# Performance work log

Hardware: AMD Instinct MI355X
Metric: run time of the kernel (lower is better)

Reference implementation:

```python
import jax, jax.numpy as jnp
import numpy as np

B, S = 4, 2000            # meshes, nodes per mesh
N = B * S                  # total nodes
E = 32000                  # directed edges (before self loops)
H_TR, D_TR, FF, TOUT = 4, 64, 2048, 16
HID, HEADS, HC = 512, 6, 512
DEFORM_IN, NUM_LOOP = 7, 3


def setup_inputs():
    key = jax.random.key(0)
    ks = iter(jax.random.split(key, 64))
    def W(shape):
        return jax.random.normal(next(ks), shape, jnp.float32) / np.sqrt(shape[-1])
    inp = {}
    inp['conv_feat'] = jax.random.normal(next(ks), (B, 1), jnp.float32)
    inp['mesh_feat'] = jax.random.normal(next(ks), (N, 4), jnp.float32)
    inp['x'] = jax.random.normal(next(ks), (N, DEFORM_IN), jnp.float32)
    inp['edge_index'] = jax.random.randint(next(ks), (2, E), 0, N, jnp.int32)
    inp['embed_w'] = W((D_TR, 4)); inp['embed_b'] = jnp.zeros((D_TR,), jnp.float32)
    inp['in_proj_w'] = W((3 * D_TR, D_TR)); inp['in_proj_b'] = jnp.zeros((3 * D_TR,), jnp.float32)
    inp['out_proj_w'] = W((D_TR, D_TR)); inp['out_proj_b'] = jnp.zeros((D_TR,), jnp.float32)
    inp['ln1_g'] = jnp.ones((D_TR,), jnp.float32); inp['ln1_b'] = jnp.zeros((D_TR,), jnp.float32)
    inp['ln2_g'] = jnp.ones((D_TR,), jnp.float32); inp['ln2_b'] = jnp.zeros((D_TR,), jnp.float32)
    inp['ff1_w'] = W((FF, D_TR)); inp['ff1_b'] = jnp.zeros((FF,), jnp.float32)
    inp['ff2_w'] = W((D_TR, FF)); inp['ff2_b'] = jnp.zeros((D_TR,), jnp.float32)
    inp['tout_w'] = W((TOUT, D_TR)); inp['tout_b'] = jnp.zeros((TOUT,), jnp.float32)
    all_feat = DEFORM_IN - 2 + TOUT  # 21
    inp['lin_w'] = W((HID, all_feat)); inp['lin_b'] = jnp.zeros((HID,), jnp.float32)
    gin = 2 + HID  # 514
    inp['gat_wl'] = W((HEADS * HC, gin)); inp['gat_bl'] = jnp.zeros((HEADS * HC,), jnp.float32)
    inp['gat_wr'] = W((HEADS * HC, gin)); inp['gat_br'] = jnp.zeros((HEADS * HC,), jnp.float32)
    inp['gat_att'] = jax.random.normal(next(ks), (HEADS, HC), jnp.float32) / np.sqrt(HC)
    inp['gat_bias'] = jnp.zeros((HC,), jnp.float32)
    inp['coord1_w'] = W((HID // 2, HID)); inp['coord1_b'] = jnp.zeros((HID // 2,), jnp.float32)
    inp['coord2_w'] = W((2, HID // 2)); inp['coord2_b'] = jnp.zeros((2,), jnp.float32)
    return inp


def _ln(h, g, b):
    m = jnp.mean(h, -1, keepdims=True)
    v = jnp.var(h, -1, keepdims=True)
    return (h - m) / jnp.sqrt(v + 1e-5) * g + b


def _mrt_forward(conv_feat, mesh_feat, x, edge_index, embed_w, embed_b, in_proj_w, in_proj_b,
                 out_proj_w, out_proj_b, ln1_g, ln1_b, ln2_g, ln2_b, ff1_w, ff1_b, ff2_w, ff2_b,
                 tout_w, tout_b, lin_w, lin_b, gat_wl, gat_bl, gat_wr, gat_br, gat_att, gat_bias,
                 coord1_w, coord1_b, coord2_w, coord2_b):
    bsz = conv_feat.shape[0]
    feat_dim = mesh_feat.shape[-1]
    # ---- transformer encoder (1 post-norm layer, eval mode => no dropout) ----
    h = mesh_feat.reshape(bsz, -1, feat_dim) @ embed_w.T + embed_b  # [B,S,D]
    qkv = h @ in_proj_w.T + in_proj_b
    q, k, v = jnp.split(qkv, 3, axis=-1)
    dh = D_TR // H_TR
    hd = lambda t: t.reshape(bsz, -1, H_TR, dh)
    attn = jax.nn.softmax(jnp.einsum('bqhd,bkhd->bhqk', hd(q), hd(k)) / np.sqrt(dh), axis=-1)
    o = jnp.einsum('bhqk,bkhd->bqhd', attn, hd(v)).reshape(bsz, -1, D_TR)
    h = _ln(h + (o @ out_proj_w.T + out_proj_b), ln1_g, ln1_b)
    ff = jax.nn.relu(h @ ff1_w.T + ff1_b) @ ff2_w.T + ff2_b
    h = _ln(h + ff, ln2_g, ln2_b)
    feats = (h @ tout_w.T + tout_b).reshape(-1, TOUT)               # [N,16]
    feats = jnp.concatenate([x[:, 2:], feats], axis=1)             # [N,21]
    hidden = jax.nn.selu(feats @ lin_w.T + lin_b)                  # [N,512]
    # ---- recurrent GATv2 deformer loop ----
    coord = x[:, :2]
    n = x.shape[0]
    loops = jnp.arange(n, dtype=edge_index.dtype)                  # self loops (GATv2Conv default)
    src = jnp.concatenate([edge_index[0], loops])
    dst = jnp.concatenate([edge_index[1], loops])
    for _ in range(NUM_LOOP):
        inp = jnp.concatenate([coord, hidden], axis=1)             # [N,514]
        xl = (inp @ gat_wl.T + gat_bl).reshape(n, HEADS, HC)
        xr = (inp @ gat_wr.T + gat_br).reshape(n, HEADS, HC)
        e = jax.nn.leaky_relu(xl[src] + xr[dst], 0.2)              # [Etot,H,C]
        logits = jnp.einsum('ehc,hc->eh', e, gat_att)              # [Etot,H]
        mx = jax.ops.segment_max(logits, dst, num_segments=n)
        a = jnp.exp(logits - mx[dst])
        a = a / jax.ops.segment_sum(a, dst, num_segments=n)[dst]   # softmax per dst node
        agg = jax.ops.segment_sum(xl[src] * a[:, :, None], dst, num_segments=n)  # [N,H,C]
        hidden = jax.nn.selu(jnp.mean(agg, axis=1) + gat_bias)     # concat=False => head mean
        coord = jax.nn.selu(hidden @ coord1_w.T + coord1_b) @ coord2_w.T + coord2_b
    return coord


def reference(conv_feat, mesh_feat, x, edge_index, embed_w, embed_b, in_proj_w, in_proj_b,
              out_proj_w, out_proj_b, ln1_g, ln1_b, ln2_g, ln2_b, ff1_w, ff1_b, ff2_w, ff2_b,
              tout_w, tout_b, lin_w, lin_b, gat_wl, gat_bl, gat_wr, gat_br, gat_att, gat_bias,
              coord1_w, coord1_b, coord2_w, coord2_b):
    return _mrt_forward(conv_feat, mesh_feat, x, edge_index, embed_w, embed_b, in_proj_w, in_proj_b,
                        out_proj_w, out_proj_b, ln1_g, ln1_b, ln2_g, ln2_b, ff1_w, ff1_b, ff2_w, ff2_b,
                        tout_w, tout_b, lin_w, lin_b, gat_wl, gat_bl, gat_wr, gat_br, gat_att, gat_bias,
                        coord1_w, coord1_b, coord2_w, coord2_b)
```

## Files before the change

### kernel.cpp

```cpp
#include <hip/hip_runtime.h>
#include <hip/hip_bf16.h>
#include <math.h>

#define NN     8000
#define MPAD   8064
#define BATCH  4
#define SEQ    2000
#define DTR    64
#define NHTR   4
#define DHD    16
#define FFD    2048
#define TOUTD  16
#define HIDD   512
#define NHEADS 6
#define HCD    512
#define GIND   514
#define GOUT   3072
#define GOUT2  6144
#define NEDGE  32000
#define ELOOP  40000

#define K1     576
#define K2     1152

#define KSPLIT 20
#define KCH    100

#define CDIV(a,b) (((a)+(b)-1)/(b))

using bf16x8 = __attribute__((__ext_vector_type__(8))) __bf16;
using f32x4  = __attribute__((__ext_vector_type__(4))) float;

__device__ __forceinline__ float selu_f(float x){
  const float a = 1.6732632423543772848f;
  const float s = 1.0507009873554805f;
  return x > 0.f ? s * x : s * a * (__expf(x) - 1.f);
}

__device__ __forceinline__ unsigned short f2bf_rn(float x){
  unsigned u = __float_as_uint(x);
  unsigned r = (u + 0x7fffu + ((u >> 16) & 1u)) >> 16;
  return (unsigned short)r;
}
__device__ __forceinline__ float bf2f(unsigned short h){
  return __uint_as_float((unsigned)h << 16);
}

template<int ACT>
__global__ __launch_bounds__(256) void k_gemm(const float* __restrict__ A,
    const float* __restrict__ W, const float* __restrict__ bias,
    float* __restrict__ C, int M, int N, int K)
{
  __shared__ float As[16][68];
  __shared__ float Ws[16][68];
  const int tid = threadIdx.x;
  const int bm = blockIdx.y * 64, bn = blockIdx.x * 64;
  const int tx = tid & 15, ty = tid >> 4;
  float acc[4][4] = {};
  for (int k0 = 0; k0 < K; k0 += 16){
    #pragma unroll
    for (int i = 0; i < 4; ++i){
      int el = tid + (i << 8);
      int kk = el & 15, r = el >> 4;
      int gk = k0 + kk;
      int gm = bm + r;
      As[kk][r] = (gm < M && gk < K) ? A[(size_t)gm * K + gk] : 0.f;
      int gn = bn + r;
      Ws[kk][r] = (gn < N && gk < K) ? W[(size_t)gn * K + gk] : 0.f;
    }
    __syncthreads();
    #pragma unroll
    for (int kk = 0; kk < 16; ++kk){
      float av[4], wv[4];
      #pragma unroll
      for (int i = 0; i < 4; ++i) av[i] = As[kk][ty*4+i];
      #pragma unroll
      for (int j = 0; j < 4; ++j) wv[j] = Ws[kk][tx*4+j];
      #pragma unroll
      for (int i = 0; i < 4; ++i)
        #pragma unroll
        for (int j = 0; j < 4; ++j) acc[i][j] = fmaf(av[i], wv[j], acc[i][j]);
    }
    __syncthreads();
  }
  #pragma unroll
  for (int i = 0; i < 4; ++i){
    int gm = bm + ty*4 + i;
    if (gm >= M) continue;
    #pragma unroll
    for (int j = 0; j < 4; ++j){
      int gn = bn + tx*4 + j;
      if (gn >= N) continue;
      float v = acc[i][j] + bias[gn];
      if (ACT == 1) v = fmaxf(v, 0.f);
      if (ACT == 2) v = selu_f(v);
      C[(size_t)gm * N + gn] = v;
    }
  }
}

__global__ __launch_bounds__(256) void k_addln4(const float* __restrict__ x,
    const float* __restrict__ part, const float* __restrict__ bias,
    const float* __restrict__ g, const float* __restrict__ b,
    float* __restrict__ out)
{
  int row = blockIdx.x * 4 + (threadIdx.x >> 6);
  int lane = threadIdx.x & 63;
  if (row >= NN) return;
  float y = bias[lane];
  #pragma unroll
  for (int z = 0; z < 4; ++z) y += part[(size_t)z*NN*DTR + (size_t)row*64 + lane];
  float v = x[(size_t)row*64 + lane] + y;
  float s1 = v, s2 = v * v;
  #pragma unroll
  for (int o = 32; o; o >>= 1){ s1 += __shfl_xor(s1, o); s2 += __shfl_xor(s2, o); }
  float mean = s1 * (1.f/64.f);
  float var  = s2 * (1.f/64.f) - mean * mean;
  float r = rsqrtf(var + 1e-5f);
  out[(size_t)row*64 + lane] = (v - mean) * r * g[lane] + b[lane];
}

__global__ __launch_bounds__(256) void k_coord2(const float* __restrict__ c1,
    const float* __restrict__ w2, const float* __restrict__ b2,
    float* __restrict__ out, short* __restrict__ abf)
{
  int n = blockIdx.x, t = threadIdx.x;
  float v = c1[(size_t)n*256 + t];
  float d0 = v * w2[t], d1 = v * w2[256 + t];
  #pragma unroll
  for (int o = 32; o; o >>= 1){ d0 += __shfl_xor(d0, o); d1 += __shfl_xor(d1, o); }
  __shared__ float red[8];
  int wv = t >> 6;
  if ((t & 63) == 0){ red[wv] = d0; red[4 + wv] = d1; }
  __syncthreads();
  if (t < 2){
    float c = (t == 0 ? red[0]+red[1]+red[2]+red[3] + b2[0]
                      : red[4]+red[5]+red[6]+red[7] + b2[1]);
    out[(size_t)n*2 + t] = c;
    abf[(size_t)n*K2 + t] = (short)f2bf_rn(c);
  }
}

__global__ void k_cvt_w(const float* __restrict__ W, short* __restrict__ Wbf)
{
  int i = blockIdx.x * blockDim.x + threadIdx.x;
  if (i >= GOUT * K1) return;
  int n = i / K1, k = i - K1 * n;
  float v = (k < GIND) ? W[(size_t)n * GIND + k] : 0.f;
  Wbf[i] = (short)f2bf_rn(v);
}

__global__ void k_cvt_wc(const float* __restrict__ W, short* __restrict__ Wbf)
{
  int i = blockIdx.x * blockDim.x + threadIdx.x;
  if (i >= 256 * K1) return;
  int n = i / K1, k = i - K1 * n;
  float v = (k >= 2 && k < GIND) ? W[(size_t)n * HIDD + (k - 2)] : 0.f;
  Wbf[i] = (short)f2bf_rn(v);
}

__global__ void k_cvt_w1(const float* __restrict__ W, short* __restrict__ Wbf)
{
  int i = blockIdx.x * blockDim.x + threadIdx.x;
  if (i >= FFD * 64) return;
  Wbf[i] = (short)f2bf_rn(W[i]);
}

__global__ void k_cvt_w2(const float* __restrict__ W, short* __restrict__ Wbf)
{
  int i = blockIdx.x * blockDim.x + threadIdx.x;
  if (i >= 128 * FFD) return;
  int n = i / FFD;
  Wbf[i] = (short)f2bf_rn(n < 64 ? W[i] : 0.f);
}

__global__ void k_cvt_h(const float* __restrict__ h, short* __restrict__ hbf)
{
  int i = blockIdx.x * blockDim.x + threadIdx.x;
  if (i >= MPAD * 64) return;
  int n = i >> 6;
  hbf[i] = (short)f2bf_rn(n < NN ? h[i] : 0.f);
}

__global__ void k_cvt_a(const float* __restrict__ coord,
                        const float* __restrict__ hidden,
                        short* __restrict__ Abf)
{
  int i = blockIdx.x * blockDim.x + threadIdx.x;
  if (i >= MPAD * K1) return;
  int n = i / K1, k = i - K1 * n;
  float v = 0.f;
  if (n < NN && k < GIND)
    v = (k < 2) ? coord[(size_t)n*2 + k] : hidden[(size_t)n*HIDD + k - 2];
  Abf[(size_t)n * K2 + k] = (short)f2bf_rn(v);
}

__global__ void k_wfuse(const float* __restrict__ ipw, const float* __restrict__ ipb,
                        const float* __restrict__ ew, const float* __restrict__ eb,
                        float* __restrict__ Wp, float* __restrict__ bp)
{
  int c = blockIdx.x * blockDim.x + threadIdx.x;
  if (c >= 192) return;
  float w4[4] = {0.f, 0.f, 0.f, 0.f};
  float bb = 0.f;
  for (int d = 0; d < 64; ++d){
    float wq = ipw[c*64 + d];
    #pragma unroll
    for (int j = 0; j < 4; ++j) w4[j] = fmaf(wq, ew[d*4 + j], w4[j]);
    bb = fmaf(wq, eb[d], bb);
  }
  #pragma unroll
  for (int j = 0; j < 4; ++j) Wp[c*4 + j] = w4[j];
  bp[c] = bb + ipb[c];
}

__global__ __launch_bounds__(256) void k_embqkv(const float* __restrict__ mesh,
    const float* __restrict__ ew, const float* __restrict__ eb,
    const float* __restrict__ Wp, const float* __restrict__ bp,
    float* __restrict__ h, float* __restrict__ qkv)
{
  int n = blockIdx.x, t = threadIdx.x;
  float m0 = mesh[n*4+0], m1 = mesh[n*4+1], m2 = mesh[n*4+2], m3 = mesh[n*4+3];
  if (t < 64){
    const float* wr = ew + t*4;
    h[(size_t)n*64 + t] =
      fmaf(m0, wr[0], fmaf(m1, wr[1], fmaf(m2, wr[2], m3*wr[3]))) + eb[t];
  } else {
    int c = t - 64;
    const float* wr = Wp + c*4;
    qkv[(size_t)n*192 + c] =
      fmaf(m0, wr[0], fmaf(m1, wr[1], fmaf(m2, wr[2], m3*wr[3]))) + bp[c];
  }
}

__global__ __launch_bounds__(256) void k_gat_mfma(
    const short* __restrict__ Abf, const short* __restrict__ Wbf,
    const float* __restrict__ bl, const float* __restrict__ br,
    unsigned short* __restrict__ Cb)
{
  __shared__ __align__(16) short smem[2 * 128 * 64];
  short* As = smem;
  short* Bs = smem + 128 * 64;
  const int tid  = threadIdx.x;
  int lin = blockIdx.y * 48 + blockIdx.x;
  int xcd = lin & 7;
  int idx = lin >> 3;
  int nb  = xcd * 6 + idx % 6;
  int mb  = idx / 6;
  const int bm = mb * 128, bn = nb * 128;
  const int w    = tid >> 6, lane = tid & 63;
  const int wr   = w >> 1, wc = w & 1;
  const int lrow = lane & 15;

  f32x4 acc[4][4];
  #pragma unroll
  for (int i = 0; i < 4; ++i)
    #pragma unroll
    for (int j = 0; j < 4; ++j) acc[i][j] = (f32x4){0.f, 0.f, 0.f, 0.f};

  for (int kt = 0; kt < 9; ++kt){
    int koff = kt * 64;
    __syncthreads();
    #pragma unroll
    for (int i = 0; i < 4; ++i){
      int l  = i * 256 + tid;
      int r  = l >> 3, j = l & 7;
      int js = j ^ (r & 7);
      const short* ga = Abf + (size_t)(bm + r) * K2 + koff + js * 8;
      const short* gb = Wbf + (size_t)(bn + r) * K1 + koff + js * 8;
      short* la = As + ((i * 256 + w * 64) << 3);
      short* lb = Bs + ((i * 256 + w * 64) << 3);
      __builtin_amdgcn_global_load_lds(
          (const __attribute__((address_space(1))) unsigned*)ga,
          (__attribute__((address_space(3))) unsigned*)la, 16, 0, 0);
      __builtin_amdgcn_global_load_lds(
          (const __attribute__((address_space(1))) unsigned*)gb,
          (__attribute__((address_space(3))) unsigned*)lb, 16, 0, 0);
    }
    __syncthreads();
    #pragma unroll
    for (int ks = 0; ks < 2; ++ks){
      const int co = ((ks * 4 + (lane >> 4)) ^ (lrow & 7)) * 8;
      bf16x8 fa[4], fb[4];
      #pragma unroll
      for (int mi = 0; mi < 4; ++mi)
        fa[mi] = *(const bf16x8*)&As[(wr*64 + mi*16 + lrow) * 64 + co];
      #pragma unroll
      for (int ni = 0; ni < 4; ++ni)
        fb[ni] = *(const bf16x8*)&Bs[(wc*64 + ni*16 + lrow) * 64 + co];
      #pragma unroll
      for (int mi = 0; mi < 4; ++mi)
        #pragma unroll
        for (int ni = 0; ni < 4; ++ni)
          acc[mi][ni] = __builtin_amdgcn_mfma_f32_16x16x32_bf16(
              fa[mi], fb[ni], acc[mi][ni], 0, 0, 0);
    }
  }
  __syncthreads();
  unsigned short* Ct = (unsigned short*)smem;
  #pragma unroll
  for (int mi = 0; mi < 4; ++mi){
    #pragma unroll
    for (int ni = 0; ni < 4; ++ni){
      int col = wc*64 + ni*16 + lrow;
      int gn  = bn + col;
      float bv = (gn < GOUT) ? bl[gn] : br[gn - GOUT];
      #pragma unroll
      for (int j = 0; j < 4; ++j){
        int row  = wr*64 + mi*16 + (lane >> 4)*4 + j;
        int colp = col ^ (((row >> 2) & 3) << 4);
        Ct[row*128 + colp] = f2bf_rn(acc[mi][ni][j] + bv);
      }
    }
  }
  __syncthreads();
  #pragma unroll
  for (int c = 0; c < 8; ++c){
    int g   = c*256 + tid;
    int row = g >> 4, cc = g & 15;
    int ccp = cc ^ (((row >> 2) & 3) << 1);
    int gm  = bm + row;
    if (gm < NN){
      bf16x8 v = *(const bf16x8*)&Ct[row*128 + ccp*8];
      *(bf16x8*)&Cb[(size_t)gm * GOUT2 + bn + cc*8] = v;
    }
  }
}

__global__ __launch_bounds__(256) void k_c1_mfma(
    const short* __restrict__ Abf, const short* __restrict__ Wbf,
    const float* __restrict__ c1b, float* __restrict__ C)
{
  __shared__ __align__(16) short smem[2 * 128 * 64];
  short* As = smem;
  short* Bs = smem + 128 * 64;
  const int tid  = threadIdx.x;
  const int bm = blockIdx.y * 128, bn = blockIdx.x * 128;
  const int w    = tid >> 6, lane = tid & 63;
  const int wr   = w >> 1, wc = w & 1;
  const int lrow = lane & 15;

  f32x4 acc[4][4];
  #pragma unroll
  for (int i = 0; i < 4; ++i)
    #pragma unroll
    for (int j = 0; j < 4; ++j) acc[i][j] = (f32x4){0.f, 0.f, 0.f, 0.f};

  for (int kt = 0; kt < 9; ++kt){
    int koff = kt * 64;
    __syncthreads();
    #pragma unroll
    for (int i = 0; i < 4; ++i){
      int l  = i * 256 + tid;
      int r  = l >> 3, j = l & 7;
      int js = j ^ (r & 7);
      const short* ga = Abf + (size_t)(bm + r) * K2 + koff + js * 8;
      const short* gb = Wbf + (size_t)(bn + r) * K1 + koff + js * 8;
      short* la = As + ((i * 256 + w * 64) << 3);
      short* lb = Bs + ((i * 256 + w * 64) << 3);
      __builtin_amdgcn_global_load_lds(
          (const __attribute__((address_space(1))) unsigned*)ga,
          (__attribute__((address_space(3))) unsigned*)la, 16, 0, 0);
      __builtin_amdgcn_global_load_lds(
          (const __attribute__((address_space(1))) unsigned*)gb,
          (__attribute__((address_space(3))) unsigned*)lb, 16, 0, 0);
    }
    __syncthreads();
    #pragma unroll
    for (int ks = 0; ks < 2; ++ks){
      const int co = ((ks * 4 + (lane >> 4)) ^ (lrow & 7)) * 8;
      bf16x8 fa[4], fb[4];
      #pragma unroll
      for (int mi = 0; mi < 4; ++mi)
        fa[mi] = *(const bf16x8*)&As[(wr*64 + mi*16 + lrow) * 64 + co];
      #pragma unroll
      for (int ni = 0; ni < 4; ++ni)
        fb[ni] = *(const bf16x8*)&Bs[(wc*64 + ni*16 + lrow) * 64 + co];
      #pragma unroll
      for (int mi = 0; mi < 4; ++mi)
        #pragma unroll
        for (int ni = 0; ni < 4; ++ni)
          acc[mi][ni] = __builtin_amdgcn_mfma_f32_16x16x32_bf16(
              fa[mi], fb[ni], acc[mi][ni], 0, 0, 0);
    }
  }
  #pragma unroll
  for (int mi = 0; mi < 4; ++mi){
    #pragma unroll
    for (int ni = 0; ni < 4; ++ni){
      int gn = bn + wc*64 + ni*16 + lrow;
      float bv = c1b[gn];
      #pragma unroll
      for (int j = 0; j < 4; ++j){
        int gm = bm + wr*64 + mi*16 + (lane >> 4) * 4 + j;
        if (gm < NN)
          C[(size_t)gm * 256 + gn] = selu_f(acc[mi][ni][j] + bv);
      }
    }
  }
}

__global__ __launch_bounds__(256) void k_ff1_mfma(
    const short* __restrict__ hbf, const short* __restrict__ w1b,
    const float* __restrict__ b1, unsigned short* __restrict__ Cb)
{
  __shared__ __align__(16) short smem[2 * 128 * 64];
  short* As = smem;
  short* Bs = smem + 128 * 64;
  const int tid  = threadIdx.x;
  const int bm = blockIdx.y * 128, bn = blockIdx.x * 128;
  const int w    = tid >> 6, lane = tid & 63;
  const int wr   = w >> 1, wc = w & 1;
  const int lrow = lane & 15;

  f32x4 acc[4][4];
  #pragma unroll
  for (int i = 0; i < 4; ++i)
    #pragma unroll
    for (int j = 0; j < 4; ++j) acc[i][j] = (f32x4){0.f, 0.f, 0.f, 0.f};

  #pragma unroll
  for (int i = 0; i < 4; ++i){
    int l  = i * 256 + tid;
    int r  = l >> 3, j = l & 7;
    int js = j ^ (r & 7);
    const short* ga = hbf + (size_t)(bm + r) * 64 + js * 8;
    const short* gb = w1b + (size_t)(bn + r) * 64 + js * 8;
    short* la = As + ((i * 256 + w * 64) << 3);
    short* lb = Bs + ((i * 256 + w * 64) << 3);
    __builtin_amdgcn_global_load_lds(
        (const __attribute__((address_space(1))) unsigned*)ga,
        (__attribute__((address_space(3))) unsigned*)la, 16, 0, 0);
    __builtin_amdgcn_global_load_lds(
        (const __attribute__((address_space(1))) unsigned*)gb,
        (__attribute__((address_space(3))) unsigned*)lb, 16, 0, 0);
  }
  __syncthreads();
  #pragma unroll
  for (int ks = 0; ks < 2; ++ks){
    const int co = ((ks * 4 + (lane >> 4)) ^ (lrow & 7)) * 8;
    bf16x8 fa[4], fb[4];
    #pragma unroll
    for (int mi = 0; mi < 4; ++mi)
      fa[mi] = *(const bf16x8*)&As[(wr*64 + mi*16 + lrow) * 64 + co];
    #pragma unroll
    for (int ni = 0; ni < 4; ++ni)
      fb[ni] = *(const bf16x8*)&Bs[(wc*64 + ni*16 + lrow) * 64 + co];
    #pragma unroll
    for (int mi = 0; mi < 4; ++mi)
      #pragma unroll
      for (int ni = 0; ni < 4; ++ni)
        acc[mi][ni] = __builtin_amdgcn_mfma_f32_16x16x32_bf16(
            fa[mi], fb[ni], acc[mi][ni], 0, 0, 0);
  }
  __syncthreads();
  unsigned short* Ct = (unsigned short*)smem;
  #pragma unroll
  for (int mi = 0; mi < 4; ++mi){
    #pragma unroll
    for (int ni = 0; ni < 4; ++ni){
      int col = wc*64 + ni*16 + lrow;
      int gn  = bn + col;
      float bv = b1[gn];
      #pragma unroll
      for (int j = 0; j < 4; ++j){
        int row  = wr*64 + mi*16 + (lane >> 4)*4 + j;
        int colp = col ^ (((row >> 2) & 3) << 4);
        Ct[row*128 + colp] = f2bf_rn(fmaxf(acc[mi][ni][j] + bv, 0.f));
      }
    }
  }
  __syncthreads();
  #pragma unroll
  for (int c = 0; c < 8; ++c){
    int g   = c*256 + tid;
    int row = g >> 4, cc = g & 15;
    int ccp = cc ^ (((row >> 2) & 3) << 1);
    int gm  = bm + row;
    if (gm < NN){
      bf16x8 v = *(const bf16x8*)&Ct[row*128 + ccp*8];
      *(bf16x8*)&Cb[(size_t)gm * FFD + bn + cc*8] = v;
    }
  }
}

__global__ __launch_bounds__(256) void k_ff2_mfma(
    const unsigned short* __restrict__ ffb, const short* __restrict__ w2b,
    float* __restrict__ part)
{
  __shared__ __align__(16) short smem[2 * 128 * 64];
  short* As = smem;
  short* Bs = smem + 128 * 64;
  const int tid  = threadIdx.x;
  const int bm = blockIdx.y * 128;
  const int kz = blockIdx.z;
  const int w    = tid >> 6, lane = tid & 63;
  const int wr   = w >> 1, wc = w & 1;
  const int lrow = lane & 15;

  f32x4 acc[4][4];
  #pragma unroll
  for (int i = 0; i < 4; ++i)
    #pragma unroll
    for (int j = 0; j < 4; ++j) acc[i][j] = (f32x4){0.f, 0.f, 0.f, 0.f};

  for (int kt = 0; kt < 8; ++kt){
    int koff = kz * 512 + kt * 64;
    __syncthreads();
    #pragma unroll
    for (int i = 0; i < 4; ++i){
      int l  = i * 256 + tid;
      int r  = l >> 3, j = l & 7;
      int js = j ^ (r & 7);
      const short* ga = (const short*)ffb + (size_t)(bm + r) * FFD + koff + js * 8;
      const short* gb = w2b + (size_t)r * FFD + koff + js * 8;
      short* la = As + ((i * 256 + w * 64) << 3);
      short* lb = Bs + ((i * 256 + w * 64) << 3);
      __builtin_amdgcn_global_load_lds(
          (const __attribute__((address_space(1))) unsigned*)ga,
          (__attribute__((address_space(3))) unsigned*)la, 16, 0, 0);
      __builtin_amdgcn_global_load_lds(
          (const __attribute__((address_space(1))) unsigned*)gb,
          (__attribute__((address_space(3))) unsigned*)lb, 16, 0, 0);
    }
    __syncthreads();
    #pragma unroll
    for (int ks = 0; ks < 2; ++ks){
      const int co = ((ks * 4 + (lane >> 4)) ^ (lrow & 7)) * 8;
      bf16x8 fa[4], fb[4];
      #pragma unroll
      for (int mi = 0; mi < 4; ++mi)
        fa[mi] = *(const bf16x8*)&As[(wr*64 + mi*16 + lrow) * 64 + co];
      #pragma unroll
      for (int ni = 0; ni < 4; ++ni)
        fb[ni] = *(const bf16x8*)&Bs[(wc*64 + ni*16 + lrow) * 64 + co];
      #pragma unroll
      for (int mi = 0; mi < 4; ++mi)
        #pragma unroll
        for (int ni = 0; ni < 4; ++ni)
          acc[mi][ni] = __builtin_amdgcn_mfma_f32_16x16x32_bf16(
              fa[mi], fb[ni], acc[mi][ni], 0, 0, 0);
    }
  }
  if (wc == 0){
    float* pz = part + (size_t)kz * NN * 64;
    #pragma unroll
    for (int mi = 0; mi < 4; ++mi){
      #pragma unroll
      for (int ni = 0; ni < 4; ++ni){
        int gn = ni*16 + lrow;
        #pragma unroll
        for (int j = 0; j < 4; ++j){
          int gm = bm + wr*64 + mi*16 + (lane >> 4) * 4 + j;
          if (gm < NN)
            pz[(size_t)gm * 64 + gn] = acc[mi][ni][j];
        }
      }
    }
  }
}

__global__ __launch_bounds__(128) void k_attn_part(const float* __restrict__ qkv,
    float* __restrict__ Pm, float* __restrict__ Pl, float* __restrict__ Pacc)
{
  __shared__ float Ks[KCH][DHD];
  __shared__ float Vs[KCH][DHD];
  const int q1 = blockIdx.x * 128 + threadIdx.x;
  const int q2 = q1 + 1024;
  const int bh = blockIdx.y;
  const int b  = bh >> 2, h = bh & 3;
  const int ks = blockIdx.z;
  const bool v2 = q2 < SEQ;
  const float SC = 0.25f * 1.4426950408889634f;
  float qv1[DHD], qv2[DHD];
  {
    const float4* qr = (const float4*)(qkv + ((size_t)(b*SEQ + q1))*192 + h*DHD);
    #pragma unroll
    for (int j = 0; j < 4; ++j){
      float4 t = qr[j];
      qv1[j*4+0] = t.x; qv1[j*4+1] = t.y; qv1[j*4+2] = t.z; qv1[j*4+3] = t.w;
    }
  }
  if (v2){
    const float4* qr = (const float4*)(qkv + ((size_t)(b*SEQ + q2))*192 + h*DHD);
    #pragma unroll
    for (int j = 0; j < 4; ++j){
      float4 t = qr[j];
      qv2[j*4+0] = t.x; qv2[j*4+1] = t.y; qv2[j*4+2] = t.z; qv2[j*4+3] = t.w;
    }
  } else {
    #pragma unroll
    for (int j = 0; j < DHD; ++j) qv2[j] = 0.f;
  }
  const int kbeg = ks * KCH;
  for (int el = threadIdx.x; el < KCH * 4; el += 128){
    int r = el >> 2, d4 = el & 3;
    const float4* base = (const float4*)(qkv + ((size_t)(b*SEQ + kbeg + r))*192 + h*DHD);
    ((float4*)Ks[r])[d4] = base[16 + d4];
    ((float4*)Vs[r])[d4] = base[32 + d4];
  }
  __syncthreads();
  float m1 = -1e30f, l1 = 0.f, a1[DHD] = {};
  float m2 = -1e30f, l2 = 0.f, a2[DHD] = {};
  for (int r = 0; r < KCH; ++r){
    float s1 = 0.f, s2 = 0.f;
    #pragma unroll
    for (int d = 0; d < DHD; ++d){
      float kd = Ks[r][d];
      s1 = fmaf(qv1[d], kd, s1);
      s2 = fmaf(qv2[d], kd, s2);
    }
    s1 *= SC; s2 *= SC;
    if (__any((s1 > m1 + 8.f) || (s2 > m2 + 8.f))){
      float mn1 = fmaxf(m1, s1), mn2 = fmaxf(m2, s2);
      float c1 = exp2f(m1 - mn1), c2 = exp2f(m2 - mn2);
      l1 *= c1; l2 *= c2;
      #pragma unroll
      for (int d = 0; d < DHD; ++d){ a1[d] *= c1; a2[d] *= c2; }
      m1 = mn1; m2 = mn2;
    }
    float p1 = exp2f(s1 - m1), p2 = exp2f(s2 - m2);
    l1 += p1; l2 += p2;
    #pragma unroll
    for (int d = 0; d < DHD; ++d){
      float vd = Vs[r][d];
      a1[d] = fmaf(p1, vd, a1[d]);
      a2[d] = fmaf(p2, vd, a2[d]);
    }
  }
  {
    size_t qi = ((size_t)bh * SEQ + q1) * KSPLIT + ks;
    Pm[qi] = m1; Pl[qi] = l1;
    #pragma unroll
    for (int d = 0; d < DHD; ++d) Pacc[qi*DHD + d] = a1[d];
  }
  if (v2){
    size_t qi = ((size_t)bh * SEQ + q2) * KSPLIT + ks;
    Pm[qi] = m2; Pl[qi] = l2;
    #pragma unroll
    for (int d = 0; d < DHD; ++d) Pacc[qi*DHD + d] = a2[d];
  }
}

__global__ void k_attn_comb(const float* __restrict__ Pm, const float* __restrict__ Pl,
                            const float* __restrict__ Pacc, float* __restrict__ o)
{
  int qi = blockIdx.x * blockDim.x + threadIdx.x;
  if (qi >= BATCH * NHTR * SEQ) return;
  float m = -1e30f;
  #pragma unroll
  for (int ks = 0; ks < KSPLIT; ++ks) m = fmaxf(m, Pm[(size_t)qi*KSPLIT + ks]);
  float l = 0.f, acc[DHD] = {};
  #pragma unroll
  for (int ks = 0; ks < KSPLIT; ++ks){
    size_t p = (size_t)qi*KSPLIT + ks;
    float sc = exp2f(Pm[p] - m);
    l += Pl[p] * sc;
    #pragma unroll
    for (int d = 0; d < DHD; ++d) acc[d] = fmaf(Pacc[p*DHD + d], sc, acc[d]);
  }
  int bh = qi / SEQ, q = qi - bh * SEQ;
  int b = bh >> 2, h = bh & 3;
  float inv = 1.f / l;
  #pragma unroll
  for (int d = 0; d < DHD; ++d)
    o[((size_t)(b*SEQ + q))*64 + h*DHD + d] = acc[d] * inv;
}

__global__ __launch_bounds__(256) void k_addln(const float* __restrict__ x,
    const float* __restrict__ y, const float* __restrict__ g,
    const float* __restrict__ b, float* __restrict__ out)
{
  int row = blockIdx.x * 4 + (threadIdx.x >> 6);
  int lane = threadIdx.x & 63;
  if (row >= NN) return;
  float v = x[(size_t)row*64 + lane] + y[(size_t)row*64 + lane];
  float s1 = v, s2 = v * v;
  #pragma unroll
  for (int o = 32; o; o >>= 1){ s1 += __shfl_xor(s1, o); s2 += __shfl_xor(s2, o); }
  float mean = s1 * (1.f/64.f);
  float var  = s2 * (1.f/64.f) - mean * mean;
  float r = rsqrtf(var + 1e-5f);
  out[(size_t)row*64 + lane] = (v - mean) * r * g[lane] + b[lane];
}

__global__ void k_prep(const float* __restrict__ x, const float* __restrict__ tout,
                       float* __restrict__ feats, float* __restrict__ coord)
{
  int i = blockIdx.x * blockDim.x + threadIdx.x;
  if (i >= NN * 23) return;
  int n = i / 23, c = i - 23*n;
  if (c < 21)
    feats[(size_t)n*21 + c] = (c < 5) ? x[(size_t)n*7 + 2 + c] : tout[(size_t)n*16 + c - 5];
  else
    coord[(size_t)n*2 + (c - 21)] = x[(size_t)n*7 + (c - 21)];
}

__global__ void k_count(const int* __restrict__ dst, int* __restrict__ cnt)
{
  int e = blockIdx.x * blockDim.x + threadIdx.x;
  if (e >= ELOOP) return;
  int d = (e < NEDGE) ? dst[e] : e - NEDGE;
  atomicAdd(&cnt[d], 1);
}

__global__ __launch_bounds__(1024) void k_scan(const int* __restrict__ cnt,
                                               int* __restrict__ ptr)
{
  __shared__ int part[1024];
  int tid = threadIdx.x;
  const int per = 8;
  int loc[per]; int s = 0;
  int base = tid * per;
  #pragma unroll
  for (int i = 0; i < per; ++i){
    int v = (base + i < NN) ? cnt[base + i] : 0;
    loc[i] = s; s += v;
  }
  part[tid] = s;
  __syncthreads();
  for (int off = 1; off < 1024; off <<= 1){
    int v = 0;
    if (tid >= off) v = part[tid - off];
    __syncthreads();
    if (tid >= off) part[tid] += v;
    __syncthreads();
  }
  int pre = tid ? part[tid - 1] : 0;
  #pragma unroll
  for (int i = 0; i < per; ++i)
    if (base + i < NN) ptr[base + i] = pre + loc[i];
  if (tid == 1023) ptr[NN] = part[1023];
}

__global__ void k_fill(const int* __restrict__ dst, const int* __restrict__ ptr,
                       int* __restrict__ fil, int* __restrict__ eid)
{
  int e = blockIdx.x * blockDim.x + threadIdx.x;
  if (e >= ELOOP) return;
  int d = (e < NEDGE) ? dst[e] : e - NEDGE;
  int pos = ptr[d] + atomicAdd(&fil[d], 1);
  eid[pos] = e;
}

__global__ __launch_bounds__(256) void k_logits(const unsigned short* __restrict__ xc,
    const int* __restrict__ src_a, const int* __restrict__ dst_a,
    const int* __restrict__ eid, const float* __restrict__ att,
    float* __restrict__ logits2)
{
  int bid = blockIdx.x;
  int wgs = (bid & 7) * 1250 + (bid >> 3);
  int pos = wgs * 4 + (threadIdx.x >> 6);
  if (pos >= ELOOP) return;
  int lane = threadIdx.x & 63;
  int e = eid[pos];
  int s = (e < NEDGE) ? src_a[e] : e - NEDGE;
  int d = (e < NEDGE) ? dst_a[e] : e - NEDGE;
  const uint4* pl = (const uint4*)(xc + (size_t)s * GOUT2);
  const uint4* pr = (const uint4*)(xc + (size_t)d * GOUT2 + GOUT);
  const float4* pa = (const float4*)att;
  #pragma unroll 2
  for (int h = 0; h < NHEADS; ++h){
    uint4 ua = pl[h*64 + lane];
    uint4 ub = pr[h*64 + lane];
    float4 w0 = pa[h*128 + lane*2], w1 = pa[h*128 + lane*2 + 1];
    float acc = 0.f;
    auto pair = [&](unsigned a, unsigned b, float wl, float wh){
      float vl = __uint_as_float(a << 16)        + __uint_as_float(b << 16);
      float vh = __uint_as_float(a & 0xffff0000u)+ __uint_as_float(b & 0xffff0000u);
      vl = vl > 0.f ? vl : 0.2f * vl;
      vh = vh > 0.f ? vh : 0.2f * vh;
      acc = fmaf(vl, wl, acc);
      acc = fmaf(vh, wh, acc);
    };
    pair(ua.x, ub.x, w0.x, w0.y);
    pair(ua.y, ub.y, w0.z, w0.w);
    pair(ua.z, ub.z, w1.x, w1.y);
    pair(ua.w, ub.w, w1.z, w1.w);
    #pragma unroll
    for (int o2 = 32; o2; o2 >>= 1) acc += __shfl_xor(acc, o2);
    if (lane == 0) logits2[pos*NHEADS + h] = acc;
  }
}

__global__ void k_stats(const float* __restrict__ logits2, const int* __restrict__ ptr,
                        float* __restrict__ mx, float* __restrict__ inv)
{
  int i = blockIdx.x * blockDim.x + threadIdx.x;
  if (i >= NN * NHEADS) return;
  int n = i / NHEADS, h = i - NHEADS * n;
  int s0 = ptr[n], s1 = ptr[n + 1];
  float m = -1e30f;
  for (int t = s0; t < s1; ++t) m = fmaxf(m, logits2[t*NHEADS + h]);
  float s = 0.f;
  for (int t = s0; t < s1; ++t) s += __expf(logits2[t*NHEADS + h] - m);
  mx[i] = m; inv[i] = 1.f / s;
}

__global__ __launch_bounds__(256) void k_agg(const unsigned short* __restrict__ xc,
    const float* __restrict__ logits2, const float* __restrict__ mx,
    const float* __restrict__ inv, const int* __restrict__ ptr,
    const int* __restrict__ eid, const int* __restrict__ src_a,
    const float* __restrict__ gbias, float* __restrict__ hidden,
    short* __restrict__ abf)
{
  const int n = blockIdx.x;
  const int tid = threadIdx.x;
  __shared__ float a_sh[64 * NHEADS];
  __shared__ int src_sh[64];
  const int s0 = ptr[n];
  const int deg = ptr[n + 1] - s0;
  float acc[12] = {};
  for (int base = 0; base < deg; base += 64){
    int cnt = min(64, deg - base);
    __syncthreads();
    for (int t = tid; t < cnt * NHEADS; t += 256){
      int ei = t / NHEADS, h = t - NHEADS * ei;
      a_sh[t] = __expf(logits2[(s0 + base + ei)*NHEADS + h] - mx[n*NHEADS + h])
                * inv[n*NHEADS + h];
      if (h == 0){
        int e = eid[s0 + base + ei];
        src_sh[ei] = (e < NEDGE) ? src_a[e] : e - NEDGE;
      }
    }
    __syncthreads();
    for (int i2 = 0; i2 < cnt; ++i2){
      const unsigned* row = (const unsigned*)(xc + (size_t)src_sh[i2] * GOUT2);
      #pragma unroll
      for (int k = 0; k < NHEADS; ++k){
        unsigned u = row[tid + (k << 8)];
        float wgt = a_sh[i2*NHEADS + k];
        acc[2*k]   = fmaf(__uint_as_float(u << 16),         wgt, acc[2*k]);
        acc[2*k+1] = fmaf(__uint_as_float(u & 0xffff0000u), wgt, acc[2*k+1]);
      }
    }
  }
  float m0 = (acc[0]+acc[2]+acc[4]+acc[6]+acc[8]+acc[10]) * (1.f/6.f);
  float m1 = (acc[1]+acc[3]+acc[5]+acc[7]+acc[9]+acc[11]) * (1.f/6.f);
  float2 out;
  out.x = selu_f(m0 + gbias[2*tid]);
  out.y = selu_f(m1 + gbias[2*tid + 1]);
  *(float2*)&hidden[(size_t)n*HIDD + 2*tid] = out;
  unsigned short h0 = f2bf_rn(out.x), h1 = f2bf_rn(out.y);
  *(unsigned*)&abf[(size_t)n*K2 + 2 + 2*tid] = (unsigned)h0 | ((unsigned)h1 << 16);
}

extern "C" void kernel_launch(void* const* d_in, const int* in_sizes, int n_in,
                              void* d_out, int out_size, void* d_ws, size_t ws_size,
                              hipStream_t stream)
{
  const float* mesh     = (const float*)d_in[1];
  const float* xin      = (const float*)d_in[2];
  const int*   ei       = (const int*)d_in[3];
  const float* embed_w  = (const float*)d_in[4];
  const float* embed_b  = (const float*)d_in[5];
  const float* in_proj_w= (const float*)d_in[6];
  const float* in_proj_b= (const float*)d_in[7];
  const float* out_proj_w=(const float*)d_in[8];
  const float* out_proj_b=(const float*)d_in[9];
  const float* ln1_g    = (const float*)d_in[10];
  const float* ln1_b    = (const float*)d_in[11];
  const float* ln2_g    = (const float*)d_in[12];
  const float* ln2_b    = (const float*)d_in[13];
  const float* ff1_w    = (const float*)d_in[14];
  const float* ff1_b    = (const float*)d_in[15];
  const float* ff2_w    = (const float*)d_in[16];
  const float* ff2_b    = (const float*)d_in[17];
  const float* tout_w   = (const float*)d_in[18];
  const float* tout_b   = (const float*)d_in[19];
  const float* lin_w    = (const float*)d_in[20];
  const float* lin_b    = (const float*)d_in[21];
  const float* gat_wl   = (const float*)d_in[22];
  const float* gat_bl   = (const float*)d_in[23];
  const float* gat_wr   = (const float*)d_in[24];
  const float* gat_br   = (const float*)d_in[25];
  const float* gat_att  = (const float*)d_in[26];
  const float* gat_bias = (const float*)d_in[27];
  const float* coord1_w = (const float*)d_in[28];
  const float* coord1_b = (const float*)d_in[29];
  const float* coord2_w = (const float*)d_in[30];
  const float* coord2_b = (const float*)d_in[31];

  const int* esrc = ei;
  const int* edst = ei + NEDGE;

  char* ws = (char*)d_ws;
  size_t off = 0;
  auto alloc = [&](size_t nbytes){
    size_t o = off; off += (nbytes + 255) & ~(size_t)255; return o;
  };
  float* hidden = (float*)(ws + alloc((size_t)NN * HIDD * 4));
  float* coord  = (float*)(ws + alloc((size_t)NN * 2 * 4));
  unsigned short* xc = (unsigned short*)(ws + alloc((size_t)NN * GOUT2 * 2));
  float* logits = (float*)(ws + alloc((size_t)ELOOP * NHEADS * 4));
  float* mxb    = (float*)(ws + alloc((size_t)NN * NHEADS * 4));
  float* invb   = (float*)(ws + alloc((size_t)NN * NHEADS * 4));
  int*   ptr    = (int*)(ws + alloc((size_t)(NN + 1) * 4));
  int*   eid    = (int*)(ws + alloc((size_t)ELOOP * 4));
  int*   cnt    = (int*)(ws + alloc((size_t)NN * 4));
  int*   fil    = (int*)(ws + alloc((size_t)NN * 4));
  short* abf    = (short*)(ws + alloc((size_t)MPAD * K2 * 2));
  short* wlbf   = (short*)(ws + alloc((size_t)GOUT * K1 * 2));
  short* wrbf   = (short*)(ws + alloc((size_t)GOUT * K1 * 2));
  short* wcb    = (short*)(ws + alloc((size_t)256 * K1 * 2));
  short* w1b    = (short*)(ws + alloc((size_t)FFD * 64 * 2));
  short* w2b    = (short*)(ws + alloc((size_t)128 * FFD * 2));
  short* hbf    = (short*)(ws + alloc((size_t)MPAD * 64 * 2));
  float* c1     = (float*)(ws + alloc((size_t)NN * 256 * 4));
  float* Wp     = (float*)(ws + alloc((size_t)192 * 4 * 4));
  float* bp     = (float*)(ws + alloc((size_t)192 * 4));

  char* arena = (char*)xc;
  float* h       = (float*)(arena + ((size_t)0  << 20));
  float* o       = (float*)(arena + ((size_t)2  << 20));
  float* tmp     = (float*)(arena + ((size_t)4  << 20));
  float* feats   = (float*)(arena + ((size_t)6  << 20));
  float* toutb   = (float*)(arena + ((size_t)7  << 20));
  float* qkv     = (float*)(arena + ((size_t)8  << 20));
  float* Pm      = (float*)(arena + ((size_t)15 << 20));
  float* Pl      = (float*)(arena + ((size_t)18 << 20));
  float* Pacc    = (float*)(arena + ((size_t)21 << 20));
  unsigned short* ffb = (unsigned short*)(arena + ((size_t)28 << 20));
  float* part_f2 = (float*)(arena + ((size_t)62 << 20));

  k_wfuse<<<1, 192, 0, stream>>>(in_proj_w, in_proj_b, embed_w, embed_b, Wp, bp);
  k_cvt_w1<<<CDIV(FFD*64, 256), 256, 0, stream>>>(ff1_w, w1b);
  k_cvt_w2<<<CDIV(128*FFD, 256), 256, 0, stream>>>(ff2_w, w2b);
  hipMemsetAsync(cnt, 0, (size_t)NN * 4, stream);
  hipMemsetAsync(fil, 0, (size_t)NN * 4, stream);
  k_count<<<CDIV(ELOOP, 256), 256, 0, stream>>>(edst, cnt);
  k_scan<<<1, 1024, 0, stream>>>(cnt, ptr);
  k_fill<<<CDIV(ELOOP, 256), 256, 0, stream>>>(edst, ptr, fil, eid);
  k_cvt_w<<<CDIV(GOUT*K1, 256), 256, 0, stream>>>(gat_wl, wlbf);
  k_cvt_w<<<CDIV(GOUT*K1, 256), 256, 0, stream>>>(gat_wr, wrbf);
  k_cvt_wc<<<CDIV(256*K1, 256), 256, 0, stream>>>(coord1_w, wcb);

  k_embqkv<<<NN, 256, 0, stream>>>(mesh, embed_w, embed_b, Wp, bp, h, qkv);
  k_attn_part<<<dim3(CDIV(SEQ,256), BATCH*NHTR, KSPLIT), 128, 0, stream>>>(qkv, Pm, Pl, Pacc);
  k_attn_comb<<<CDIV(BATCH*NHTR*SEQ, 256), 256, 0, stream>>>(Pm, Pl, Pacc, o);
  k_gemm<0><<<dim3(1, CDIV(NN,64)), 256, 0, stream>>>(o, out_proj_w, out_proj_b, tmp, NN, 64, 64);
  k_addln<<<CDIV(NN,4), 256, 0, stream>>>(h, tmp, ln1_g, ln1_b, h);
  k_cvt_h<<<CDIV(MPAD*64, 256), 256, 0, stream>>>(h, hbf);
  k_ff1_mfma<<<dim3(16, 63), 256, 0, stream>>>(hbf, w1b, ff1_b, ffb);
  k_ff2_mfma<<<dim3(1, 63, 4), 256, 0, stream>>>(ffb, w2b, part_f2);
  k_addln4<<<CDIV(NN,4), 256, 0, stream>>>(h, part_f2, ff2_b, ln2_g, ln2_b, h);
  k_gemm<0><<<dim3(1, CDIV(NN,64)), 256, 0, stream>>>(h, tout_w, tout_b, toutb, NN, TOUTD, DTR);
  k_prep<<<CDIV(NN*23, 256), 256, 0, stream>>>(xin, toutb, feats, coord);
  k_gemm<2><<<dim3(CDIV(HIDD,64), CDIV(NN,64)), 256, 0, stream>>>(feats, lin_w, lin_b, hidden, NN, HIDD, 21);
  k_cvt_a<<<CDIV(MPAD*K1, 256), 256, 0, stream>>>(coord, hidden, abf);

  for (int it = 0; it < 3; ++it){
    k_gat_mfma<<<dim3(48, 63), 256, 0, stream>>>(abf, wlbf, gat_bl, gat_br, xc);
    k_logits<<<ELOOP/4, 256, 0, stream>>>(xc, esrc, edst, eid, gat_att, logits);
    k_stats<<<CDIV(NN*NHEADS, 256), 256, 0, stream>>>(logits, ptr, mxb, invb);
    k_agg<<<NN, 256, 0, stream>>>(xc, logits, mxb, invb, ptr, eid, esrc, gat_bias, hidden, abf);
    k_c1_mfma<<<dim3(2, 63), 256, 0, stream>>>(abf, wcb, coord1_b, c1);
    float* cdst = (it == 2) ? (float*)d_out : coord;
    k_coord2<<<NN, 256, 0, stream>>>(c1, coord2_w, coord2_b, cdst, abf);
  }
}
```

Before: 801.6 us.

## Fuse GAT logits, softmax stats and aggregation into one online-softmax kernel

Replaces the three GAT kernels (edge logits, per-node max/sum stats, weighted aggregation) with a single per-destination-node kernel. It computes logits on the fly from the gathered source row and the resident dst row, then applies an online softmax. This removes the logits, max and inverse-sum intermediate buffers, two launches per iteration and the second read of source rows. The cost is two block-wide barriers per edge for the cross-wave logit reduction, which serialises work inside each block. Separately, the bf16 conversion of h is folded into the first add+layernorm, and the padding rows are zeroed once.

```diff
diff --git a/kernel.cpp b/kernel.cpp
--- a/kernel.cpp
+++ b/kernel.cpp
@@ -174,14 +174,6 @@
   Wbf[i] = (short)f2bf_rn(n < 64 ? W[i] : 0.f);
 }
 
-__global__ void k_cvt_h(const float* __restrict__ h, short* __restrict__ hbf)
-{
-  int i = blockIdx.x * blockDim.x + threadIdx.x;
-  if (i >= MPAD * 64) return;
-  int n = i >> 6;
-  hbf[i] = (short)f2bf_rn(n < NN ? h[i] : 0.f);
-}
-
 __global__ void k_cvt_a(const float* __restrict__ coord,
                         const float* __restrict__ hidden,
                         short* __restrict__ Abf)
@@ -669,7 +661,8 @@
 
 __global__ __launch_bounds__(256) void k_addln(const float* __restrict__ x,
     const float* __restrict__ y, const float* __restrict__ g,
-    const float* __restrict__ b, float* __restrict__ out)
+    const float* __restrict__ b, float* __restrict__ out,
+    short* __restrict__ hbf)
 {
   int row = blockIdx.x * 4 + (threadIdx.x >> 6);
   int lane = threadIdx.x & 63;
@@ -681,7 +674,9 @@
   float mean = s1 * (1.f/64.f);
   float var  = s2 * (1.f/64.f) - mean * mean;
   float r = rsqrtf(var + 1e-5f);
-  out[(size_t)row*64 + lane] = (v - mean) * r * g[lane] + b[lane];
+  float res = (v - mean) * r * g[lane] + b[lane];
+  out[(size_t)row*64 + lane] = res;
+  hbf[(size_t)row*64 + lane] = (short)f2bf_rn(res);
 }
 
 __global__ void k_prep(const float* __restrict__ x, const float* __restrict__ tout,
@@ -696,6 +691,13 @@
     coord[(size_t)n*2 + (c - 21)] = x[(size_t)n*7 + (c - 21)];
 }
 
+__global__ void k_zpad(short* __restrict__ hbf)
+{
+  int i = blockIdx.x * blockDim.x + threadIdx.x;
+  if (i >= (MPAD - NN) * 64) return;
+  hbf[(size_t)NN*64 + i] = 0;
+}
+
 __global__ void k_count(const int* __restrict__ dst, int* __restrict__ cnt)
 {
   int e = blockIdx.x * blockDim.x + threadIdx.x;
@@ -743,103 +745,90 @@
   eid[pos] = e;
 }
 
-__global__ __launch_bounds__(256) void k_logits(const unsigned short* __restrict__ xc,
-    const int* __restrict__ src_a, const int* __restrict__ dst_a,
-    const int* __restrict__ eid, const float* __restrict__ att,
-    float* __restrict__ logits2)
-{
-  int bid = blockIdx.x;
-  int wgs = (bid & 7) * 1250 + (bid >> 3);
-  int pos = wgs * 4 + (threadIdx.x >> 6);
-  if (pos >= ELOOP) return;
-  int lane = threadIdx.x & 63;
-  int e = eid[pos];
-  int s = (e < NEDGE) ? src_a[e] : e - NEDGE;
-  int d = (e < NEDGE) ? dst_a[e] : e - NEDGE;
-  const uint4* pl = (const uint4*)(xc + (size_t)s * GOUT2);
-  const uint4* pr = (const uint4*)(xc + (size_t)d * GOUT2 + GOUT);
-  const float4* pa = (const float4*)att;
-  #pragma unroll 2
-  for (int h = 0; h < NHEADS; ++h){
-    uint4 ua = pl[h*64 + lane];
-    uint4 ub = pr[h*64 + lane];
-    float4 w0 = pa[h*128 + lane*2], w1 = pa[h*128 + lane*2 + 1];
-    float acc = 0.f;
-    auto pair = [&](unsigned a, unsigned b, float wl, float wh){
-      float vl = __uint_as_float(a << 16)        + __uint_as_float(b << 16);
-      float vh = __uint_as_float(a & 0xffff0000u)+ __uint_as_float(b & 0xffff0000u);
-      vl = vl > 0.f ? vl : 0.2f * vl;
-      vh = vh > 0.f ? vh : 0.2f * vh;
-      acc = fmaf(vl, wl, acc);
-      acc = fmaf(vh, wh, acc);
-    };
-    pair(ua.x, ub.x, w0.x, w0.y);
-    pair(ua.y, ub.y, w0.z, w0.w);
-    pair(ua.z, ub.z, w1.x, w1.y);
-    pair(ua.w, ub.w, w1.z, w1.w);
-    #pragma unroll
-    for (int o2 = 32; o2; o2 >>= 1) acc += __shfl_xor(acc, o2);
-    if (lane == 0) logits2[pos*NHEADS + h] = acc;
-  }
-}
-
-__global__ void k_stats(const float* __restrict__ logits2, const int* __restrict__ ptr,
-                        float* __restrict__ mx, float* __restrict__ inv)
-{
-  int i = blockIdx.x * blockDim.x + threadIdx.x;
-  if (i >= NN * NHEADS) return;
-  int n = i / NHEADS, h = i - NHEADS * n;
-  int s0 = ptr[n], s1 = ptr[n + 1];
-  float m = -1e30f;
-  for (int t = s0; t < s1; ++t) m = fmaxf(m, logits2[t*NHEADS + h]);
-  float s = 0.f;
-  for (int t = s0; t < s1; ++t) s += __expf(logits2[t*NHEADS + h] - m);
-  mx[i] = m; inv[i] = 1.f / s;
-}
-
-__global__ __launch_bounds__(256) void k_agg(const unsigned short* __restrict__ xc,
-    const float* __restrict__ logits2, const float* __restrict__ mx,
-    const float* __restrict__ inv, const int* __restrict__ ptr,
-    const int* __restrict__ eid, const int* __restrict__ src_a,
+__global__ __launch_bounds__(256) void k_aggf(const unsigned short* __restrict__ xc,
+    const int* __restrict__ ptr, const int* __restrict__ eid,
+    const int* __restrict__ src_a, const float* __restrict__ att,
     const float* __restrict__ gbias, float* __restrict__ hidden,
     short* __restrict__ abf)
 {
   const int n = blockIdx.x;
   const int tid = threadIdx.x;
-  __shared__ float a_sh[64 * NHEADS];
-  __shared__ int src_sh[64];
+  const int lane = tid & 63, wv = tid >> 6;
+  __shared__ int   src_sh[64];
+  __shared__ float redl[24];
   const int s0 = ptr[n];
   const int deg = ptr[n + 1] - s0;
-  float acc[12] = {};
+
+  float xr0[6], xr1[6], at0[6], at1[6];
+  const unsigned* xrrow = (const unsigned*)(xc + (size_t)n * GOUT2 + GOUT);
+  #pragma unroll
+  for (int k = 0; k < 6; ++k){
+    unsigned ur = xrrow[tid + (k << 8)];
+    xr0[k] = __uint_as_float(ur << 16);
+    xr1[k] = __uint_as_float(ur & 0xffff0000u);
+    at0[k] = att[k*512 + 2*tid];
+    at1[k] = att[k*512 + 2*tid + 1];
+  }
+  float mh[6], lh[6], acc[12];
+  #pragma unroll
+  for (int k = 0; k < 6; ++k){ mh[k] = -1e30f; lh[k] = 0.f; }
+  #pragma unroll
+  for (int j = 0; j < 12; ++j) acc[j] = 0.f;
+
   for (int base = 0; base < deg; base += 64){
     int cnt = min(64, deg - base);
     __syncthreads();
-    for (int t = tid; t < cnt * NHEADS; t += 256){
-      int ei = t / NHEADS, h = t - NHEADS * ei;
-      a_sh[t] = __expf(logits2[(s0 + base + ei)*NHEADS + h] - mx[n*NHEADS + h])
-                * inv[n*NHEADS + h];
-      if (h == 0){
-        int e = eid[s0 + base + ei];
-        src_sh[ei] = (e < NEDGE) ? src_a[e] : e - NEDGE;
-      }
+    if (tid < cnt){
+      int e = eid[s0 + base + tid];
+      src_sh[tid] = (e < NEDGE) ? src_a[e] : e - NEDGE;
     }
     __syncthreads();
     for (int i2 = 0; i2 < cnt; ++i2){
       const unsigned* row = (const unsigned*)(xc + (size_t)src_sh[i2] * GOUT2);
-      #pragma unroll
-      for (int k = 0; k < NHEADS; ++k){
-        unsigned u = row[tid + (k << 8)];
-        float wgt = a_sh[i2*NHEADS + k];
-        acc[2*k]   = fmaf(__uint_as_float(u << 16),         wgt, acc[2*k]);
-        acc[2*k+1] = fmaf(__uint_as_float(u & 0xffff0000u), wgt, acc[2*k+1]);
+      unsigned u[6];
+      float part[6];
+      #pragma unroll
+      for (int k = 0; k < 6; ++k){
+        unsigned uu = row[tid + (k << 8)];
+        u[k] = uu;
+        float v0 = __uint_as_float(uu << 16)         + xr0[k];
+        float v1 = __uint_as_float(uu & 0xffff0000u) + xr1[k];
+        v0 = v0 > 0.f ? v0 : 0.2f * v0;
+        v1 = v1 > 0.f ? v1 : 0.2f * v1;
+        part[k] = fmaf(v0, at0[k], v1 * at1[k]);
       }
-    }
-  }
-  float m0 = (acc[0]+acc[2]+acc[4]+acc[6]+acc[8]+acc[10]) * (1.f/6.f);
-  float m1 = (acc[1]+acc[3]+acc[5]+acc[7]+acc[9]+acc[11]) * (1.f/6.f);
+      #pragma unroll
+      for (int k = 0; k < 6; ++k){
+        float p = part[k];
+        #pragma unroll
+        for (int o2 = 32; o2; o2 >>= 1) p += __shfl_xor(p, o2);
+        if (lane == 0) redl[wv*6 + k] = p;
+      }
+      __syncthreads();
+      #pragma unroll
+      for (int k = 0; k < 6; ++k){
+        float lg = redl[k] + redl[6 + k] + redl[12 + k] + redl[18 + k];
+        float mn = fmaxf(mh[k], lg);
+        float sc = __expf(mh[k] - mn);
+        float w  = __expf(lg - mn);
+        lh[k] = fmaf(lh[k], sc, w);
+        acc[2*k]   = fmaf(acc[2*k],   sc, w * __uint_as_float(u[k] << 16));
+        acc[2*k+1] = fmaf(acc[2*k+1], sc, w * __uint_as_float(u[k] & 0xffff0000u));
+        mh[k] = mn;
+      }
+      __syncthreads();
+    }
+  }
+  float s0a = 0.f, s1a = 0.f;
+  #pragma unroll
+  for (int k = 0; k < 6; ++k){
+    float inv = 1.f / lh[k];
+    s0a = fmaf(acc[2*k],   inv, s0a);
+    s1a = fmaf(acc[2*k+1], inv, s1a);
+  }
   float2 out;
-  out.x = selu_f(m0 + gbias[2*tid]);
-  out.y = selu_f(m1 + gbias[2*tid + 1]);
+  out.x = selu_f(s0a * (1.f/6.f) + gbias[2*tid]);
+  out.y = selu_f(s1a * (1.f/6.f) + gbias[2*tid + 1]);
   *(float2*)&hidden[(size_t)n*HIDD + 2*tid] = out;
   unsigned short h0 = f2bf_rn(out.x), h1 = f2bf_rn(out.y);
   *(unsigned*)&abf[(size_t)n*K2 + 2 + 2*tid] = (unsigned)h0 | ((unsigned)h1 << 16);
@@ -892,9 +881,6 @@
   float* hidden = (float*)(ws + alloc((size_t)NN * HIDD * 4));
   float* coord  = (float*)(ws + alloc((size_t)NN * 2 * 4));
   unsigned short* xc = (unsigned short*)(ws + alloc((size_t)NN * GOUT2 * 2));
-  float* logits = (float*)(ws + alloc((size_t)ELOOP * NHEADS * 4));
-  float* mxb    = (float*)(ws + alloc((size_t)NN * NHEADS * 4));
-  float* invb   = (float*)(ws + alloc((size_t)NN * NHEADS * 4));
   int*   ptr    = (int*)(ws + alloc((size_t)(NN + 1) * 4));
   int*   eid    = (int*)(ws + alloc((size_t)ELOOP * 4));
   int*   cnt    = (int*)(ws + alloc((size_t)NN * 4));
@@ -926,6 +912,7 @@
   k_wfuse<<<1, 192, 0, stream>>>(in_proj_w, in_proj_b, embed_w, embed_b, Wp, bp);
   k_cvt_w1<<<CDIV(FFD*64, 256), 256, 0, stream>>>(ff1_w, w1b);
   k_cvt_w2<<<CDIV(128*FFD, 256), 256, 0, stream>>>(ff2_w, w2b);
+  k_zpad<<<CDIV((MPAD-NN)*64, 256), 256, 0, stream>>>(hbf);
   hipMemsetAsync(cnt, 0, (size_t)NN * 4, stream);
   hipMemsetAsync(fil, 0, (size_t)NN * 4, stream);
   k_count<<<CDIV(ELOOP, 256), 256, 0, stream>>>(edst, cnt);
@@ -939,8 +926,7 @@
   k_attn_part<<<dim3(CDIV(SEQ,256), BATCH*NHTR, KSPLIT), 128, 0, stream>>>(qkv, Pm, Pl, Pacc);
   k_attn_comb<<<CDIV(BATCH*NHTR*SEQ, 256), 256, 0, stream>>>(Pm, Pl, Pacc, o);
   k_gemm<0><<<dim3(1, CDIV(NN,64)), 256, 0, stream>>>(o, out_proj_w, out_proj_b, tmp, NN, 64, 64);
-  k_addln<<<CDIV(NN,4), 256, 0, stream>>>(h, tmp, ln1_g, ln1_b, h);
-  k_cvt_h<<<CDIV(MPAD*64, 256), 256, 0, stream>>>(h, hbf);
+  k_addln<<<CDIV(NN,4), 256, 0, stream>>>(h, tmp, ln1_g, ln1_b, h, hbf);
   k_ff1_mfma<<<dim3(16, 63), 256, 0, stream>>>(hbf, w1b, ff1_b, ffb);
   k_ff2_mfma<<<dim3(1, 63, 4), 256, 0, stream>>>(ffb, w2b, part_f2);
   k_addln4<<<CDIV(NN,4), 256, 0, stream>>>(h, part_f2, ff2_b, ln2_g, ln2_b, h);
@@ -951,9 +937,7 @@
 
   for (int it = 0; it < 3; ++it){
     k_gat_mfma<<<dim3(48, 63), 256, 0, stream>>>(abf, wlbf, gat_bl, gat_br, xc);
-    k_logits<<<ELOOP/4, 256, 0, stream>>>(xc, esrc, edst, eid, gat_att, logits);
-    k_stats<<<CDIV(NN*NHEADS, 256), 256, 0, stream>>>(logits, ptr, mxb, invb);
-    k_agg<<<NN, 256, 0, stream>>>(xc, logits, mxb, invb, ptr, eid, esrc, gat_bias, hidden, abf);
+    k_aggf<<<NN, 256, 0, stream>>>(xc, ptr, eid, esrc, gat_att, gat_bias, hidden, abf);
     k_c1_mfma<<<dim3(2, 63), 256, 0, stream>>>(abf, wcb, coord1_b, c1);
     float* cdst = (it == 2) ? (float*)d_out : coord;
     k_coord2<<<NN, 256, 0, stream>>>(c1, coord2_w, coord2_b, cdst, abf);
```

New measurement: 932.0 us. 16.3% more time.
